# Optimization experiments

Hardware: AMD Instinct MI355X
Metric: run time of the kernel (lower is better)

Reference implementation:

```python
import jax, jax.numpy as jnp
import numpy as np

B, T, V, H, L = 2048, 128, 256, 20, 15  # batch, seq_len, vocab, hidden, max_label


def setup_inputs() -> dict:
    key = jax.random.key(0)
    ks = jax.random.split(key, 8)
    g = lambda k, shape, s: (jax.random.normal(k, shape, jnp.float32) * s)
    return {
        "x": jax.random.randint(ks[0], (B, T), 0, V, dtype=jnp.int32),
        "W0": g(ks[1], (V, 3 * H), 0.06),   # input kernel layer 0 [V, 3H] (z|r|h)
        "U0": g(ks[2], (H, 3 * H), 0.2),    # recurrent kernel layer 0
        "b0i": jnp.zeros((3 * H,), jnp.float32),  # input bias (reset_after=True split bias)
        "b0r": jnp.zeros((3 * H,), jnp.float32),  # recurrent bias
        "W1": g(ks[3], (H, 3 * H), 0.2),
        "U1": g(ks[4], (H, 3 * H), 0.2),
        "b1i": jnp.zeros((3 * H,), jnp.float32),
        "b1r": jnp.zeros((3 * H,), jnp.float32),
        "Wd": g(ks[5], (H, L), 0.2),
        "bd": jnp.zeros((L,), jnp.float32),
        "drop_rate": 0,  # identity dropout (deterministic reference)
    }


def _gru_cell(h, xw, U, br):
    # Keras GRUCell with reset_after=True:
    #   xw = x @ W + b_in  (precomputed), rec = h @ U + b_rec
    rec = h @ U + br
    xz, xr, xh = jnp.split(xw, 3, axis=-1)
    rz, rr, rh = jnp.split(rec, 3, axis=-1)
    z = jax.nn.sigmoid(xz + rz)
    r = jax.nn.sigmoid(xr + rr)
    hh = jnp.tanh(xh + r * rh)
    return z * h + (1.0 - z) * hh


def reference(x, W0, U0, b0i, b0r, W1, U1, b1i, b1r, Wd, bd, drop_rate):
    # one_hot(x) @ W0 == gather rows of W0 (same math, no [B,T,V] materialization)
    xW0 = W0[x] + b0i                 # [B, T, 3H]
    xW0 = jnp.swapaxes(xW0, 0, 1)     # [T, B, 3H] for scan over time

    def step(carry, xw_t):
        h0, h1 = carry
        h0 = _gru_cell(h0, xw_t, U0, b0r)
        xw1 = h0 @ W1 + b1i
        h1 = _gru_cell(h1, xw1, U1, b1r)
        return (h0, h1), None

    h0 = jnp.zeros((x.shape[0], H), W0.dtype)
    h1 = jnp.zeros((x.shape[0], H), W0.dtype)
    (h0, h1), _ = jax.lax.scan(step, (h0, h1), xW0)
    # tf.nn.dropout with rate 0 is the identity
    out = h1
    logits = jax.nn.softmax(out @ Wd + bd, axis=-1)  # [B, L]
    return logits
```

## Files before the change

### kernel.cpp

```cpp
#include <hip/hip_runtime.h>


#define BB 2048
#define TT 128
#define HH 20
#define LL 15
#define H3 60

typedef float v2f __attribute__((ext_vector_type(2)));

__device__ __forceinline__ float bclane(float v, int k) {
    return __int_as_float(__builtin_amdgcn_readlane(__float_as_int(v), k));
}
__device__ __forceinline__ float bperm(int byteaddr, float v) {
    return __int_as_float(__builtin_amdgcn_ds_bpermute(byteaddr, __float_as_int(v)));
}
__device__ __forceinline__ float fast_rcp(float x) { return __builtin_amdgcn_rcpf(x); }
__device__ __forceinline__ float sigm(float x) { return fast_rcp(1.f + __expf(-x)); }
__device__ __forceinline__ float tanh_f(float x) { return 1.f - 2.f * fast_rcp(1.f + __expf(2.f * x)); }
#define PIN(v) asm volatile("" : "+v"(v))

extern "C" __global__ __launch_bounds__(256)
__attribute__((amdgpu_waves_per_eu(2, 2)))
void gru2_kernel(const int* __restrict__ x, const float* __restrict__ W0,
                 const float* __restrict__ U0, const float* __restrict__ b0i,
                 const float* __restrict__ b0r, const float* __restrict__ W1,
                 const float* __restrict__ U1, const float* __restrict__ b1i,
                 const float* __restrict__ b1r, const float* __restrict__ Wd,
                 const float* __restrict__ bd, float* __restrict__ out)
{
    const int lane = threadIdx.x & 63;
    const int w = threadIdx.x >> 6;
    const int b = blockIdx.x * 4 + w;
    const int c = lane < H3 ? lane : H3 - 1;

    __shared__ __align__(16) float hbuf[4][2][24];
    float* h0buf = &hbuf[w][0][0];
    float* h1buf = &hbuf[w][1][0];
    if (lane >= 40 && lane < H3) { h0buf[lane - 40] = 0.f; h1buf[lane - 40] = 0.f; }

    v2f u0p[HH / 2], u1p[HH / 2];
    float w1c[HH];
#pragma unroll
    for (int p = 0; p < HH / 2; ++p) {
        u0p[p] = v2f{U0[(2 * p) * H3 + c], U0[(2 * p + 1) * H3 + c]};
        u1p[p] = v2f{U1[(2 * p) * H3 + c], U1[(2 * p + 1) * H3 + c]};
    }
#pragma unroll
    for (int k = 0; k < HH; ++k) w1c[k] = W1[k * H3 + c];
#pragma unroll
    for (int p = 0; p < HH / 2; ++p) { PIN(u0p[p]); PIN(u1p[p]); }
#pragma unroll
    for (int k = 0; k < HH; ++k) PIN(w1c[k]);
    float bi0 = b0i[c], br0 = b0r[c], bi1 = b1i[c], br1 = b1r[c];
    PIN(bi0); PIN(br0); PIN(bi1); PIN(br1);

    const int* xrow = x + b * TT;
    const int tokA = xrow[lane];
    const int tokB = xrow[64 + lane];

    const int aR = ((lane - 20) & 63) << 2;
    const int aZ = ((lane - 40) & 63) << 2;

    float h0 = 0.f, h1 = 0.f;

    const int tok0 = __builtin_amdgcn_readlane(tokA, 0);
    const int tok1 = __builtin_amdgcn_readlane(tokA, 1);
    int tokn2 = __builtin_amdgcn_readlane(tokA, 2);
    float xw_cur = W0[tok0 * H3 + c] + bi0;
    float xw_nxt = W0[tok1 * H3 + c];

#pragma unroll 2
    for (int t = 0; t < TT; ++t) {
        const int t3 = (t + 3 < TT) ? (t + 3) : (TT - 1);
        const float xw_pf = W0[tokn2 * H3 + c];
        const int tokn3 = __builtin_amdgcn_readlane(t3 < 64 ? tokA : tokB, t3 & 63);

        const float4* h0q = (const float4*)h0buf;
        v2f a0 = v2f{br0, 0.f};
#pragma unroll
        for (int q = 0; q < 5; ++q) {
            const float4 hv = h0q[q];
            a0 = __builtin_elementwise_fma(v2f{hv.x, hv.y}, u0p[2 * q], a0);
            a0 = __builtin_elementwise_fma(v2f{hv.z, hv.w}, u0p[2 * q + 1], a0);
        }
        const float rec0 = a0.x + a0.y;

        const float sg0 = sigm(xw_cur + rec0);
        const float rv0 = bperm(aR, sg0);
        const float zv0 = bperm(aZ, sg0);
        const float hh0 = tanh_f(xw_cur + rv0 * rec0);
        h0 = fmaf(zv0, h0 - hh0, hh0);

        if (lane >= 40 && lane < H3) h0buf[lane - 40] = h0;

        const float4* h1q = (const float4*)h1buf;
        v2f a1 = v2f{br1, 0.f};
#pragma unroll
        for (int q = 0; q < 5; ++q) {
            const float4 hv = h1q[q];
            a1 = __builtin_elementwise_fma(v2f{hv.x, hv.y}, u1p[2 * q], a1);
            a1 = __builtin_elementwise_fma(v2f{hv.z, hv.w}, u1p[2 * q + 1], a1);
        }
        const float rec1 = a1.x + a1.y;

        float xa = bi1, xb = 0.f;
#pragma unroll
        for (int k = 0; k < 10; ++k) xa = fmaf(bclane(h0, 40 + k), w1c[k], xa);
#pragma unroll
        for (int k = 10; k < HH; ++k) xb = fmaf(bclane(h0, 40 + k), w1c[k], xb);
        const float xw1 = xa + xb;

        const float sg1 = sigm(xw1 + rec1);
        const float rv1 = bperm(aR, sg1);
        const float zv1 = bperm(aZ, sg1);
        const float hh1 = tanh_f(xw1 + rv1 * rec1);
        h1 = fmaf(zv1, h1 - hh1, hh1);

        if (lane >= 40 && lane < H3) h1buf[lane - 40] = h1;

        xw_cur = xw_nxt + bi0;
        xw_nxt = xw_pf;
        tokn2 = tokn3;
    }

    const int l = lane < LL ? lane : LL - 1;
    float acc = bd[l];
#pragma unroll
    for (int k = 0; k < HH; ++k)
        acc = fmaf(bclane(h1, 40 + k), Wd[k * LL + l], acc);

    float m = acc;
#pragma unroll
    for (int i = 0; i < LL; ++i) m = fmaxf(m, bclane(acc, i));
    const float e = __expf(acc - m);
    float s = 0.f;
#pragma unroll
    for (int i = 0; i < LL; ++i) s += bclane(e, i);
    const float p = e * fast_rcp(s);

    if (lane < LL) out[b * LL + lane] = p;
}

extern "C" void kernel_launch(void* const* d_in, const int* in_sizes, int n_in,
                              void* d_out, int out_size, void* d_ws, size_t ws_size,
                              hipStream_t stream) {
    const int*   x   = (const int*)  d_in[0];
    const float* W0  = (const float*)d_in[1];
    const float* U0  = (const float*)d_in[2];
    const float* b0i = (const float*)d_in[3];
    const float* b0r = (const float*)d_in[4];
    const float* W1  = (const float*)d_in[5];
    const float* U1  = (const float*)d_in[6];
    const float* b1i = (const float*)d_in[7];
    const float* b1r = (const float*)d_in[8];
    const float* Wd  = (const float*)d_in[9];
    const float* bd  = (const float*)d_in[10];
    float* out = (float*)d_out;

    dim3 grid(BB / 4), block(256);
    hipLaunchKernelGGL(gru2_kernel, grid, block, 0, stream,
                       x, W0, U0, b0i, b0r, W1, U1, b1i, b1r, Wd, bd, out);
}
```

Measured before the change: 143.0 us.

## Skew GRU layers across timesteps and interleave gate lanes for DPP shuffles

```diff
diff --git a/kernel.cpp b/kernel.cpp
--- a/kernel.cpp
+++ b/kernel.cpp
@@ -12,13 +12,15 @@
 __device__ __forceinline__ float bclane(float v, int k) {
     return __int_as_float(__builtin_amdgcn_readlane(__float_as_int(v), k));
 }
-__device__ __forceinline__ float bperm(int byteaddr, float v) {
-    return __int_as_float(__builtin_amdgcn_ds_bpermute(byteaddr, __float_as_int(v)));
+__device__ __forceinline__ float dpp_rshr1(float v) {
+    return __int_as_float(__builtin_amdgcn_update_dpp(
+        0, __float_as_int(v), 0x111, 0xF, 0xF, true));
 }
 __device__ __forceinline__ float fast_rcp(float x) { return __builtin_amdgcn_rcpf(x); }
 __device__ __forceinline__ float sigm(float x) { return fast_rcp(1.f + __expf(-x)); }
 __device__ __forceinline__ float tanh_f(float x) { return 1.f - 2.f * fast_rcp(1.f + __expf(2.f * x)); }
 #define PIN(v) asm volatile("" : "+v"(v))
+#define LDSFENCE() asm volatile("" ::: "memory")
 
 extern "C" __global__ __launch_bounds__(256)
 __attribute__((amdgpu_waves_per_eu(2, 2)))
@@ -32,103 +34,135 @@
     const int lane = threadIdx.x & 63;
     const int w = threadIdx.x >> 6;
     const int b = blockIdx.x * 4 + w;
-    const int c = lane < H3 ? lane : H3 - 1;
+    const int row = lane >> 4;
+    const int pos = lane & 15;
+    const int pc  = (pos < 15) ? pos : 14;
+    const int u   = pc / 3;
+    const int p3  = pc % 3;
+    const int j   = row * 5 + u;
+    const bool home = (pos < 15) && (p3 == 2);
+    const int col = p3 * 20 + j;
 
     __shared__ __align__(16) float hbuf[4][2][24];
     float* h0buf = &hbuf[w][0][0];
     float* h1buf = &hbuf[w][1][0];
-    if (lane >= 40 && lane < H3) { h0buf[lane - 40] = 0.f; h1buf[lane - 40] = 0.f; }
+    if (home) { h0buf[j] = 0.f; h1buf[j] = 0.f; }
+    LDSFENCE();
 
-    v2f u0p[HH / 2], u1p[HH / 2];
-    float w1c[HH];
+    v2f u0p[10], w1p[10], u1p[10];
 #pragma unroll
-    for (int p = 0; p < HH / 2; ++p) {
-        u0p[p] = v2f{U0[(2 * p) * H3 + c], U0[(2 * p + 1) * H3 + c]};
-        u1p[p] = v2f{U1[(2 * p) * H3 + c], U1[(2 * p + 1) * H3 + c]};
+    for (int q = 0; q < 10; ++q) {
+        const int k0 = (2 * q) * H3, k1 = (2 * q + 1) * H3;
+        u0p[q] = v2f{U0[k0 + col], U0[k1 + col]};
+        w1p[q] = v2f{W1[k0 + col], W1[k1 + col]};
+        u1p[q] = v2f{U1[k0 + col], U1[k1 + col]};
     }
 #pragma unroll
-    for (int k = 0; k < HH; ++k) w1c[k] = W1[k * H3 + c];
-#pragma unroll
-    for (int p = 0; p < HH / 2; ++p) { PIN(u0p[p]); PIN(u1p[p]); }
-#pragma unroll
-    for (int k = 0; k < HH; ++k) PIN(w1c[k]);
-    float bi0 = b0i[c], br0 = b0r[c], bi1 = b1i[c], br1 = b1r[c];
+    for (int q = 0; q < 10; ++q) { PIN(u0p[q]); PIN(w1p[q]); PIN(u1p[q]); }
+    float bi0 = b0i[col], br0 = b0r[col], bi1 = b1i[col], br1 = b1r[col];
     PIN(bi0); PIN(br0); PIN(bi1); PIN(br1);
 
     const int* xrow = x + b * TT;
     const int tokA = xrow[lane];
     const int tokB = xrow[64 + lane];
 
-    const int aR = ((lane - 20) & 63) << 2;
-    const int aZ = ((lane - 40) & 63) << 2;
-
     float h0 = 0.f, h1 = 0.f;
 
     const int tok0 = __builtin_amdgcn_readlane(tokA, 0);
     const int tok1 = __builtin_amdgcn_readlane(tokA, 1);
     int tokn2 = __builtin_amdgcn_readlane(tokA, 2);
-    float xw_cur = W0[tok0 * H3 + c] + bi0;
-    float xw_nxt = W0[tok1 * H3 + c];
+    float xw_cur = W0[tok0 * H3 + col] + bi0;
+    float xw_nxt = W0[tok1 * H3 + col];
+
+    {
+        const float pf = W0[tokn2 * H3 + col];
+        const int tokn3 = __builtin_amdgcn_readlane(tokA, 3);
+        const float rec0 = br0;
+        const float sg0 = sigm(xw_cur + rec0);
+        const float rv0 = dpp_rshr1(sg0);
+        const float zv0 = dpp_rshr1(rv0);
+        const float hh0 = tanh_f(xw_cur + rv0 * rec0);
+        h0 = fmaf(zv0, h0 - hh0, hh0);
+        if (home) h0buf[j] = h0;
+        LDSFENCE();
+        xw_cur = xw_nxt + bi0; xw_nxt = pf; tokn2 = tokn3;
+    }
 
 #pragma unroll 2
-    for (int t = 0; t < TT; ++t) {
-        const int t3 = (t + 3 < TT) ? (t + 3) : (TT - 1);
-        const float xw_pf = W0[tokn2 * H3 + c];
+    for (int i = 1; i < TT; ++i) {
+        const int t3 = (i + 3 < TT) ? (i + 3) : (TT - 1);
+        const float pf = W0[tokn2 * H3 + col];
         const int tokn3 = __builtin_amdgcn_readlane(t3 < 64 ? tokA : tokB, t3 & 63);
 
         const float4* h0q = (const float4*)h0buf;
+        const float4* h1q = (const float4*)h1buf;
         v2f a0 = v2f{br0, 0.f};
+        v2f a1 = v2f{bi1, 0.f};
+        v2f a2 = v2f{br1, 0.f};
 #pragma unroll
         for (int q = 0; q < 5; ++q) {
-            const float4 hv = h0q[q];
-            a0 = __builtin_elementwise_fma(v2f{hv.x, hv.y}, u0p[2 * q], a0);
-            a0 = __builtin_elementwise_fma(v2f{hv.z, hv.w}, u0p[2 * q + 1], a0);
+            const float4 hv0 = h0q[q];
+            const float4 hv1 = h1q[q];
+            const v2f hA = v2f{hv0.x, hv0.y}, hB = v2f{hv0.z, hv0.w};
+            const v2f gA = v2f{hv1.x, hv1.y}, gB = v2f{hv1.z, hv1.w};
+            a0 = __builtin_elementwise_fma(hA, u0p[2 * q], a0);
+            a0 = __builtin_elementwise_fma(hB, u0p[2 * q + 1], a0);
+            a1 = __builtin_elementwise_fma(hA, w1p[2 * q], a1);
+            a1 = __builtin_elementwise_fma(hB, w1p[2 * q + 1], a1);
+            a2 = __builtin_elementwise_fma(gA, u1p[2 * q], a2);
+            a2 = __builtin_elementwise_fma(gB, u1p[2 * q + 1], a2);
         }
         const float rec0 = a0.x + a0.y;
+        const float xw1  = a1.x + a1.y;
+        const float rec1 = a2.x + a2.y;
 
         const float sg0 = sigm(xw_cur + rec0);
-        const float rv0 = bperm(aR, sg0);
-        const float zv0 = bperm(aZ, sg0);
+        const float rv0 = dpp_rshr1(sg0);
+        const float zv0 = dpp_rshr1(rv0);
         const float hh0 = tanh_f(xw_cur + rv0 * rec0);
         h0 = fmaf(zv0, h0 - hh0, hh0);
+        if (home) h0buf[j] = h0;
+        LDSFENCE();
 
-        if (lane >= 40 && lane < H3) h0buf[lane - 40] = h0;
+        const float sg1 = sigm(xw1 + rec1);
+        const float rv1 = dpp_rshr1(sg1);
+        const float zv1 = dpp_rshr1(rv1);
+        const float hh1 = tanh_f(xw1 + rv1 * rec1);
+        h1 = fmaf(zv1, h1 - hh1, hh1);
+        if (home) h1buf[j] = h1;
+        LDSFENCE();
 
+        xw_cur = xw_nxt + bi0; xw_nxt = pf; tokn2 = tokn3;
+    }
+
+    {
+        const float4* h0q = (const float4*)h0buf;
         const float4* h1q = (const float4*)h1buf;
-        v2f a1 = v2f{br1, 0.f};
+        v2f a1 = v2f{bi1, 0.f}, a2 = v2f{br1, 0.f};
 #pragma unroll
         for (int q = 0; q < 5; ++q) {
-            const float4 hv = h1q[q];
-            a1 = __builtin_elementwise_fma(v2f{hv.x, hv.y}, u1p[2 * q], a1);
-            a1 = __builtin_elementwise_fma(v2f{hv.z, hv.w}, u1p[2 * q + 1], a1);
+            const float4 hv0 = h0q[q];
+            const float4 hv1 = h1q[q];
+            a1 = __builtin_elementwise_fma(v2f{hv0.x, hv0.y}, w1p[2 * q], a1);
+            a1 = __builtin_elementwise_fma(v2f{hv0.z, hv0.w}, w1p[2 * q + 1], a1);
+            a2 = __builtin_elementwise_fma(v2f{hv1.x, hv1.y}, u1p[2 * q], a2);
+            a2 = __builtin_elementwise_fma(v2f{hv1.z, hv1.w}, u1p[2 * q + 1], a2);
         }
-        const float rec1 = a1.x + a1.y;
-
-        float xa = bi1, xb = 0.f;
-#pragma unroll
-        for (int k = 0; k < 10; ++k) xa = fmaf(bclane(h0, 40 + k), w1c[k], xa);
-#pragma unroll
-        for (int k = 10; k < HH; ++k) xb = fmaf(bclane(h0, 40 + k), w1c[k], xb);
-        const float xw1 = xa + xb;
-
+        const float xw1 = a1.x + a1.y, rec1 = a2.x + a2.y;
         const float sg1 = sigm(xw1 + rec1);
-        const float rv1 = bperm(aR, sg1);
-        const float zv1 = bperm(aZ, sg1);
+        const float rv1 = dpp_rshr1(sg1);
+        const float zv1 = dpp_rshr1(rv1);
         const float hh1 = tanh_f(xw1 + rv1 * rec1);
         h1 = fmaf(zv1, h1 - hh1, hh1);
-
-        if (lane >= 40 && lane < H3) h1buf[lane - 40] = h1;
-
-        xw_cur = xw_nxt + bi0;
-        xw_nxt = xw_pf;
-        tokn2 = tokn3;
+        if (home) h1buf[j] = h1;
+        LDSFENCE();
     }
 
     const int l = lane < LL ? lane : LL - 1;
     float acc = bd[l];
 #pragma unroll
     for (int k = 0; k < HH; ++k)
-        acc = fmaf(bclane(h1, 40 + k), Wd[k * LL + l], acc);
+        acc = fmaf(h1buf[k], Wd[k * LL + l], acc);
 
     float m = acc;
 #pragma unroll
@@ -137,9 +171,9 @@
     float s = 0.f;
 #pragma unroll
     for (int i = 0; i < LL; ++i) s += bclane(e, i);
-    const float p = e * fast_rcp(s);
+    const float pr = e * fast_rcp(s);
 
-    if (lane < LL) out[b * LL + lane] = p;
+    if (lane < LL) out[b * LL + lane] = pr;
 }
 
 extern "C" void kernel_launch(void* const* d_in, const int* in_sizes, int n_in,
```

Result: faster. 125.3 us (-12.4%).
